# Kernel optimization log

Measured on AMD Instinct MI355X. Metric: run time of the kernel, lower is better.

The kernel has to match this reference:

```python
import jax, jax.numpy as jnp
import numpy as np

H = 1024   # hidden_dim
D = 256    # dynamics_dim
L = 2      # gru layers
BS = 1024  # batch
T = 256    # max_len
# activation layout over D: softmax[0:32], softmax[32:47], sigmoid[47:48], sigmoid[48:256]
CAT1 = 32
CAT2_SM_END = 47

def setup_inputs():
    key = jax.random.key(0)
    ks = jax.random.split(key, 12)
    s = 0.02
    return {
        "embed": jax.random.normal(ks[0], (BS, H * (1 + L)), jnp.float32),
        "dynamics": jax.random.uniform(ks[1], (BS, T, D), jnp.float32),
        "seq_len": T,
        "W_ih0": s * jax.random.normal(ks[2], (3 * H, H + D), jnp.float32),
        "W_hh0": s * jax.random.normal(ks[3], (3 * H, H), jnp.float32),
        "b_ih0": s * jax.random.normal(ks[4], (3 * H,), jnp.float32),
        "b_hh0": s * jax.random.normal(ks[5], (3 * H,), jnp.float32),
        "W_ih1": s * jax.random.normal(ks[6], (3 * H, H), jnp.float32),
        "W_hh1": s * jax.random.normal(ks[7], (3 * H, H), jnp.float32),
        "b_ih1": s * jax.random.normal(ks[8], (3 * H,), jnp.float32),
        "b_hh1": s * jax.random.normal(ks[9], (3 * H,), jnp.float32),
        "W_fc": s * jax.random.normal(ks[10], (D, H), jnp.float32),
        "b_fc": s * jax.random.normal(ks[11], (D,), jnp.float32),
    }

def gru_cell(inp, h, W_ih, W_hh, b_ih, b_hh):
    # PyTorch GRU cell math
    gi = inp @ W_ih.T + b_ih          # (bs, 3H)
    gh = h @ W_hh.T + b_hh            # (bs, 3H)
    r = jax.nn.sigmoid(gi[:, :H] + gh[:, :H])
    z = jax.nn.sigmoid(gi[:, H:2 * H] + gh[:, H:2 * H])
    n = jnp.tanh(gi[:, 2 * H:] + r * gh[:, 2 * H:])
    return (1.0 - z) * n + z * h

def apply_activation(x):
    # mirrors processors layout: cat(32), cat-missing(15 softmax + 1 sigmoid), cont(208 sigmoid)
    return jnp.concatenate([
        jax.nn.softmax(x[:, :CAT1], axis=-1),
        jax.nn.softmax(x[:, CAT1:CAT2_SM_END], axis=-1),
        jax.nn.sigmoid(x[:, CAT2_SM_END:]),
    ], axis=-1)

def reference(embed, dynamics, seq_len, W_ih0, W_hh0, b_ih0, b_hh0,
              W_ih1, W_hh1, b_ih1, b_hh1, W_fc, b_fc):
    glob = embed[:, :H]                      # (bs, H)
    h0 = embed[:, H:2 * H]                   # layer-0 initial hidden
    h1 = embed[:, 2 * H:3 * H]               # layer-1 initial hidden
    x0 = dynamics[:, 0, :]                   # (bs, D)

    def step(carry, _):
        x, h0, h1 = carry
        inp = jnp.concatenate([glob, jax.lax.stop_gradient(x)], axis=-1)  # x.detach()
        h0n = gru_cell(inp, h0, W_ih0, W_hh0, b_ih0, b_hh0)
        h1n = gru_cell(h0n, h1, W_ih1, W_hh1, b_ih1, b_hh1)
        out = apply_activation(h1n @ W_fc.T + b_fc)  # (bs, D)
        return (out, h0n, h1n), out

    _, res = jax.lax.scan(step, (x0, h0, h1), None, length=T)
    res = jnp.transpose(res, (1, 0, 2))  # (bs, max_len, D)
    return res
```

## Files before the change

kernel.cpp:

```cpp
#include <hip/hip_runtime.h>

#define HH    1024
#define DD    256
#define BSB   1024
#define TT    256
#define N3H   3072
#define CAT1  32
#define CAT2E 47

typedef unsigned short u16;
typedef short bf16x8 __attribute__((ext_vector_type(8)));
typedef float f32x4  __attribute__((ext_vector_type(4)));

__device__ __forceinline__ u16 f2bf(float f) {
  unsigned int x = __float_as_uint(f);
  unsigned int lsb = (x >> 16) & 1u;
  x += 0x7fffu + lsb;
  return (u16)(x >> 16);
}

__device__ __forceinline__ void gload_lds16(const u16* src, u16* lds) {
  __builtin_amdgcn_global_load_lds(
      (const __attribute__((address_space(1))) void*)src,
      (__attribute__((address_space(3))) void*)lds, 16, 0, 0);
}

struct GArg {
  const u16* A; int lda; int K;
  const u16* B; int ldb; int N;
  float* C; int ldc;
  const float* bias;
  const float* addend;
  float* out;
  u16* xout;
  int tstep;
  int act;
};

#define BM 128
#define BN 128
#define BK 64

__global__ __launch_bounds__(256, 2) void gemm_bt4(GArg ga, GArg gb)
{
  GArg g = (blockIdx.z == 0) ? ga : gb;
  const int colBase = blockIdx.x * BN;
  if (colBase >= g.N) return;
  const int rowBase = blockIdx.y * BM;

  __shared__ __align__(16) u16 As[2][BM * BK];
  __shared__ __align__(16) u16 Bs[2][BN * BK];

  const int tid  = threadIdx.x;
  const int wave = tid >> 6;
  const int lane = tid & 63;
  const int q    = lane >> 4;
  const int l16  = lane & 15;
  const int waveRow = (wave >> 1) * 64;
  const int waveCol = (wave & 1) * 64;

  const int  srow = wave * 8 + (lane >> 3);
  const int  sswz = ((lane & 7) ^ (lane >> 3)) << 3;
  const u16* aptr = g.A + (size_t)(rowBase + srow) * g.lda + sswz;
  const u16* bptr = g.B + (size_t)(colBase + srow) * g.ldb + sswz;
  const size_t astep = (size_t)32 * g.lda;
  const size_t bstep = (size_t)32 * g.ldb;
  const int ldoff = wave << 9;

  f32x4 acc[4][4];
  #pragma unroll
  for (int i = 0; i < 4; ++i)
    #pragma unroll
    for (int j = 0; j < 4; ++j)
      acc[i][j] = (f32x4){0.f, 0.f, 0.f, 0.f};

  const int nk = g.K >> 6;

  #pragma unroll
  for (int i = 0; i < 4; ++i) {
    gload_lds16(aptr + (size_t)i * astep, &As[0][ldoff + (i << 11)]);
    gload_lds16(bptr + (size_t)i * bstep, &Bs[0][ldoff + (i << 11)]);
  }
  #pragma unroll
  for (int i = 0; i < 4; ++i) {
    gload_lds16(aptr + 64 + (size_t)i * astep, &As[1][ldoff + (i << 11)]);
    gload_lds16(bptr + 64 + (size_t)i * bstep, &Bs[1][ldoff + (i << 11)]);
  }

  for (int k = 0; k < nk; ++k) {
    const int cur = k & 1;
    if (k < nk - 1) {
      asm volatile("s_waitcnt vmcnt(8)" ::: "memory");
    } else {
      asm volatile("s_waitcnt vmcnt(0)" ::: "memory");
    }
    __builtin_amdgcn_s_barrier();
    __builtin_amdgcn_sched_barrier(0);

    #pragma unroll
    for (int ks = 0; ks < 2; ++ks) {
      bf16x8 af[4], bfr[4];
      const int kb = (ks << 2) + q;
      #pragma unroll
      for (int mi = 0; mi < 4; ++mi) {
        int r = waveRow + mi * 16 + l16;
        af[mi] = *(const bf16x8*)&As[cur][(r << 6) + ((kb ^ (l16 & 7)) << 3)];
      }
      #pragma unroll
      for (int ni = 0; ni < 4; ++ni) {
        int r = waveCol + ni * 16 + l16;
        bfr[ni] = *(const bf16x8*)&Bs[cur][(r << 6) + ((kb ^ (l16 & 7)) << 3)];
      }
      #pragma unroll
      for (int mi = 0; mi < 4; ++mi)
        #pragma unroll
        for (int ni = 0; ni < 4; ++ni)
          acc[mi][ni] = __builtin_amdgcn_mfma_f32_16x16x32_bf16(af[mi], bfr[ni], acc[mi][ni], 0, 0, 0);
    }

    __builtin_amdgcn_sched_barrier(0);
    __builtin_amdgcn_s_barrier();
    __builtin_amdgcn_sched_barrier(0);
    if (k + 2 < nk) {
      const int k2 = (k + 2) << 6;
      #pragma unroll
      for (int i = 0; i < 4; ++i) {
        gload_lds16(aptr + k2 + (size_t)i * astep, &As[cur][ldoff + (i << 11)]);
        gload_lds16(bptr + k2 + (size_t)i * bstep, &Bs[cur][ldoff + (i << 11)]);
      }
    }
  }

  if (g.act) {
    const bool smWave = (colBase + waveCol) == 0;
    #pragma unroll
    for (int mi = 0; mi < 4; ++mi) {
      #pragma unroll
      for (int r = 0; r < 4; ++r) {
        const int row = rowBase + waveRow + mi * 16 + q * 4 + r;
        float v[4];
        #pragma unroll
        for (int ni = 0; ni < 4; ++ni)
          v[ni] = acc[mi][ni][r] + g.bias[colBase + waveCol + ni * 16 + l16];
        float res[4];
        if (smWave) {
          float m1 = fmaxf(v[0], v[1]);
          #pragma unroll
          for (int msk = 1; msk < 16; msk <<= 1) m1 = fmaxf(m1, __shfl_xor(m1, msk));
          float e0 = expf(v[0] - m1), e1 = expf(v[1] - m1);
          float s1 = e0 + e1;
          #pragma unroll
          for (int msk = 1; msk < 16; msk <<= 1) s1 += __shfl_xor(s1, msk);
          res[0] = e0 / s1;
          res[1] = e1 / s1;
          float mv = (l16 < 15) ? v[2] : -1e30f;
          #pragma unroll
          for (int msk = 1; msk < 16; msk <<= 1) mv = fmaxf(mv, __shfl_xor(mv, msk));
          float e2 = expf(v[2] - mv);
          float sv = (l16 < 15) ? e2 : 0.f;
          #pragma unroll
          for (int msk = 1; msk < 16; msk <<= 1) sv += __shfl_xor(sv, msk);
          res[2] = (l16 < 15) ? (e2 / sv) : (1.f / (1.f + expf(-v[2])));
          res[3] = 1.f / (1.f + expf(-v[3]));
        } else {
          #pragma unroll
          for (int ni = 0; ni < 4; ++ni)
            res[ni] = 1.f / (1.f + expf(-v[ni]));
        }
        #pragma unroll
        for (int ni = 0; ni < 4; ++ni) {
          const int col = colBase + waveCol + ni * 16 + l16;
          g.out[((size_t)row * TT + g.tstep) * DD + col] = res[ni];
          g.xout[row * DD + col] = f2bf(res[ni]);
        }
      }
    }
    return;
  }

  #pragma unroll
  for (int mi = 0; mi < 4; ++mi) {
    #pragma unroll
    for (int ni = 0; ni < 4; ++ni) {
      #pragma unroll
      for (int r = 0; r < 4; ++r) {
        int row = rowBase + waveRow + mi * 16 + q * 4 + r;
        int col = colBase + waveCol + ni * 16 + l16;
        float v = acc[mi][ni][r];
        if (g.bias)   v += g.bias[col];
        if (g.addend) v += g.addend[(size_t)row * g.ldc + col];
        g.C[(size_t)row * g.ldc + col] = v;
      }
    }
  }
}

__device__ __forceinline__ float gate1f(float gir, float ghr, float giz, float ghz,
                                        float gin, float ghn, float hv) {
  float r = 1.f / (1.f + expf(-(gir + ghr)));
  float z = 1.f / (1.f + expf(-(giz + ghz)));
  float n = tanhf(gin + r * ghn);
  return (1.f - z) * n + z * hv;
}

__global__ void gate_kernel(const float4* __restrict__ GI, const float4* __restrict__ GH,
                            float4* __restrict__ h, ushort4* __restrict__ hbf)
{
  int idx = blockIdx.x * blockDim.x + threadIdx.x;
  int b = idx >> 8, m = idx & 255;
  size_t base = (size_t)b * 768;
  float4 gir = GI[base + m], giz = GI[base + 256 + m], gin = GI[base + 512 + m];
  float4 ghr = GH[base + m], ghz = GH[base + 256 + m], ghn = GH[base + 512 + m];
  float4 hv = h[idx];
  float4 hn;
  hn.x = gate1f(gir.x, ghr.x, giz.x, ghz.x, gin.x, ghn.x, hv.x);
  hn.y = gate1f(gir.y, ghr.y, giz.y, ghz.y, gin.y, ghn.y, hv.y);
  hn.z = gate1f(gir.z, ghr.z, giz.z, ghz.z, gin.z, ghn.z, hv.z);
  hn.w = gate1f(gir.w, ghr.w, giz.w, ghz.w, gin.w, ghn.w, hv.w);
  h[idx] = hn;
  ushort4 hb;
  hb.x = f2bf(hn.x); hb.y = f2bf(hn.y); hb.z = f2bf(hn.z); hb.w = f2bf(hn.w);
  hbf[idx] = hb;
}

__global__ void convert_kernel(const float* __restrict__ src, u16* __restrict__ dst, int n)
{
  int i = blockIdx.x * blockDim.x + threadIdx.x;
  if (i < n) dst[i] = f2bf(src[i]);
}

__global__ void prep_state(const float* __restrict__ embed, const float* __restrict__ dyn,
                           u16* __restrict__ globbf,
                           float* __restrict__ h0, u16* __restrict__ h0bf,
                           float* __restrict__ h1, u16* __restrict__ h1bf,
                           u16* __restrict__ xbf)
{
  int idx = blockIdx.x * blockDim.x + threadIdx.x;
  int b = idx >> 10, j = idx & 1023;
  const float* e = embed + (size_t)b * 3072;
  globbf[idx] = f2bf(e[j]);
  float v0 = e[1024 + j]; h0[idx] = v0; h0bf[idx] = f2bf(v0);
  float v1 = e[2048 + j]; h1[idx] = v1; h1bf[idx] = f2bf(v1);
  if (j < DD) {
    xbf[b * DD + j] = f2bf(dyn[(size_t)b * (TT * DD) + j]);
  }
}

extern "C" void kernel_launch(void* const* d_in, const int* in_sizes, int n_in,
                              void* d_out, int out_size, void* d_ws, size_t ws_size,
                              hipStream_t stream)
{
  const float* embed = (const float*)d_in[0];
  const float* dyn   = (const float*)d_in[1];
  const float* W_ih0 = (const float*)d_in[3];
  const float* W_hh0 = (const float*)d_in[4];
  const float* b_ih0 = (const float*)d_in[5];
  const float* b_hh0 = (const float*)d_in[6];
  const float* W_ih1 = (const float*)d_in[7];
  const float* W_hh1 = (const float*)d_in[8];
  const float* b_ih1 = (const float*)d_in[9];
  const float* b_hh1 = (const float*)d_in[10];
  const float* W_fc  = (const float*)d_in[11];
  const float* b_fc  = (const float*)d_in[12];
  float* out = (float*)d_out;

  char* ws = (char*)d_ws;
  size_t off = 0;
  auto carve = [&](size_t bytes) -> void* {
    void* p = ws + off;
    off += (bytes + 255) & ~(size_t)255;
    return p;
  };
  u16* Wih0b = (u16*)carve((size_t)N3H * 1280 * 2);
  u16* Whh0b = (u16*)carve((size_t)N3H * HH * 2);
  u16* Wih1b = (u16*)carve((size_t)N3H * HH * 2);
  u16* Whh1b = (u16*)carve((size_t)N3H * HH * 2);
  u16* Wfcb  = (u16*)carve((size_t)DD * HH * 2);
  u16* globb = (u16*)carve((size_t)BSB * HH * 2);
  u16* xbf   = (u16*)carve((size_t)BSB * DD * 2);
  float* h0f = (float*)carve((size_t)BSB * HH * 4);
  float* h1f = (float*)carve((size_t)BSB * HH * 4);
  u16* h0b   = (u16*)carve((size_t)BSB * HH * 2);
  u16* h1b   = (u16*)carve((size_t)BSB * HH * 2);
  float* Gglob  = (float*)carve((size_t)BSB * N3H * 4);
  float* GI     = (float*)carve((size_t)BSB * N3H * 4);
  float* GH0f   = (float*)carve((size_t)BSB * N3H * 4);
  float* GH1f   = (float*)carve((size_t)BSB * N3H * 4);
  (void)ws_size;

  {
    int n;
    n = N3H * 1280; convert_kernel<<<(n + 255) / 256, 256, 0, stream>>>(W_ih0, Wih0b, n);
    n = N3H * HH;   convert_kernel<<<(n + 255) / 256, 256, 0, stream>>>(W_hh0, Whh0b, n);
    n = N3H * HH;   convert_kernel<<<(n + 255) / 256, 256, 0, stream>>>(W_ih1, Wih1b, n);
    n = N3H * HH;   convert_kernel<<<(n + 255) / 256, 256, 0, stream>>>(W_hh1, Whh1b, n);
    n = DD * HH;    convert_kernel<<<(n + 255) / 256, 256, 0, stream>>>(W_fc, Wfcb, n);
  }
  prep_state<<<(BSB * HH) / 256, 256, 0, stream>>>(embed, dyn, globb, h0f, h0b, h1f, h1b, xbf);

  const dim3 G1(N3H / BN, BSB / BM, 1);
  const dim3 G2(N3H / BN, BSB / BM, 2);

  {
    GArg g{globb, HH, HH, Wih0b, 1280, N3H, Gglob, N3H, b_ih0, nullptr, nullptr, nullptr, 0, 0};
    gemm_bt4<<<G1, 256, 0, stream>>>(g, g);
  }
  {
    GArg ga{h0b, HH, HH, Whh0b, HH, N3H, GH0f, N3H, b_hh0, nullptr, nullptr, nullptr, 0, 0};
    GArg gb{h1b, HH, HH, Whh1b, HH, N3H, GH1f, N3H, b_hh1, nullptr, nullptr, nullptr, 0, 0};
    gemm_bt4<<<G2, 256, 0, stream>>>(ga, gb);
  }
  {
    GArg g{xbf, DD, DD, Wih0b + HH, 1280, N3H, GI, N3H, nullptr, Gglob, nullptr, nullptr, 0, 0};
    gemm_bt4<<<G1, 256, 0, stream>>>(g, g);
  }

  for (int t = 0; t < TT; ++t) {
    bool last = (t == TT - 1);

    gate_kernel<<<(BSB * HH / 4) / 256, 256, 0, stream>>>(
        (const float4*)GI, (const float4*)GH0f, (float4*)h0f, (ushort4*)h0b);

    {
      GArg gi{h0b, HH, HH, Wih1b, HH, N3H, GI, N3H, b_ih1, nullptr, nullptr, nullptr, 0, 0};
      GArg gh{h0b, HH, HH, Whh0b, HH, N3H, GH0f, N3H, b_hh0, nullptr, nullptr, nullptr, 0, 0};
      gemm_bt4<<<last ? G1 : G2, 256, 0, stream>>>(gi, gh);
    }

    gate_kernel<<<(BSB * HH / 4) / 256, 256, 0, stream>>>(
        (const float4*)GI, (const float4*)GH1f, (float4*)h1f, (ushort4*)h1b);

    {
      GArg gc{h1b, HH, HH, Wfcb, HH, DD, nullptr, DD, b_fc, nullptr, out, xbf, t, 1};
      GArg gh{h1b, HH, HH, Whh1b, HH, N3H, GH1f, N3H, b_hh1, nullptr, nullptr, nullptr, 0, 0};
      gemm_bt4<<<last ? G1 : G2, 256, 0, stream>>>(gc, gh);
    }

    if (!last) {
      GArg g{xbf, DD, DD, Wih0b + HH, 1280, N3H, GI, N3H, nullptr, Gglob, nullptr, nullptr, 0, 0};
      gemm_bt4<<<G1, 256, 0, stream>>>(g, g);
    }
  }
}
```

Baseline: 25.10 ms.

## Fuse GRU gate nonlinearity into the input-projection GEMM epilogue

```diff
diff --git a/kernel.cpp b/kernel.cpp
--- a/kernel.cpp
+++ b/kernel.cpp
@@ -41,15 +41,14 @@
 #define BN 128
 #define BK 64
 
-__global__ __launch_bounds__(256, 2) void gemm_bt4(GArg ga, GArg gb)
-{
-  GArg g = (blockIdx.z == 0) ? ga : gb;
+__device__ void plain_gemm_body(const GArg& g, u16* lds)
+{
   const int colBase = blockIdx.x * BN;
   if (colBase >= g.N) return;
   const int rowBase = blockIdx.y * BM;
 
-  __shared__ __align__(16) u16 As[2][BM * BK];
-  __shared__ __align__(16) u16 Bs[2][BN * BK];
+  u16* As = lds;
+  u16* Bs = lds + 16384;
 
   const int tid  = threadIdx.x;
   const int wave = tid >> 6;
@@ -78,17 +77,17 @@
 
   #pragma unroll
   for (int i = 0; i < 4; ++i) {
-    gload_lds16(aptr + (size_t)i * astep, &As[0][ldoff + (i << 11)]);
-    gload_lds16(bptr + (size_t)i * bstep, &Bs[0][ldoff + (i << 11)]);
+    gload_lds16(aptr + (size_t)i * astep, &As[ldoff + (i << 11)]);
+    gload_lds16(bptr + (size_t)i * bstep, &Bs[ldoff + (i << 11)]);
   }
   #pragma unroll
   for (int i = 0; i < 4; ++i) {
-    gload_lds16(aptr + 64 + (size_t)i * astep, &As[1][ldoff + (i << 11)]);
-    gload_lds16(bptr + 64 + (size_t)i * bstep, &Bs[1][ldoff + (i << 11)]);
+    gload_lds16(aptr + 64 + (size_t)i * astep, &As[8192 + ldoff + (i << 11)]);
+    gload_lds16(bptr + 64 + (size_t)i * bstep, &Bs[8192 + ldoff + (i << 11)]);
   }
 
   for (int k = 0; k < nk; ++k) {
-    const int cur = k & 1;
+    const int cb = (k & 1) << 13;
     if (k < nk - 1) {
       asm volatile("s_waitcnt vmcnt(8)" ::: "memory");
     } else {
@@ -104,12 +103,12 @@
       #pragma unroll
       for (int mi = 0; mi < 4; ++mi) {
         int r = waveRow + mi * 16 + l16;
-        af[mi] = *(const bf16x8*)&As[cur][(r << 6) + ((kb ^ (l16 & 7)) << 3)];
+        af[mi] = *(const bf16x8*)&As[cb + (r << 6) + ((kb ^ (l16 & 7)) << 3)];
       }
       #pragma unroll
       for (int ni = 0; ni < 4; ++ni) {
         int r = waveCol + ni * 16 + l16;
-        bfr[ni] = *(const bf16x8*)&Bs[cur][(r << 6) + ((kb ^ (l16 & 7)) << 3)];
+        bfr[ni] = *(const bf16x8*)&Bs[cb + (r << 6) + ((kb ^ (l16 & 7)) << 3)];
       }
       #pragma unroll
       for (int mi = 0; mi < 4; ++mi)
@@ -125,8 +124,8 @@
       const int k2 = (k + 2) << 6;
       #pragma unroll
       for (int i = 0; i < 4; ++i) {
-        gload_lds16(aptr + k2 + (size_t)i * astep, &As[cur][ldoff + (i << 11)]);
-        gload_lds16(bptr + k2 + (size_t)i * bstep, &Bs[cur][ldoff + (i << 11)]);
+        gload_lds16(aptr + k2 + (size_t)i * astep, &As[cb + ldoff + (i << 11)]);
+        gload_lds16(bptr + k2 + (size_t)i * bstep, &Bs[cb + ldoff + (i << 11)]);
       }
     }
   }
@@ -195,32 +194,158 @@
   }
 }
 
-__device__ __forceinline__ float gate1f(float gir, float ghr, float giz, float ghz,
-                                        float gin, float ghn, float hv) {
-  float r = 1.f / (1.f + expf(-(gir + ghr)));
-  float z = 1.f / (1.f + expf(-(giz + ghz)));
-  float n = tanhf(gin + r * ghn);
-  return (1.f - z) * n + z * hv;
-}
-
-__global__ void gate_kernel(const float4* __restrict__ GI, const float4* __restrict__ GH,
-                            float4* __restrict__ h, ushort4* __restrict__ hbf)
-{
-  int idx = blockIdx.x * blockDim.x + threadIdx.x;
-  int b = idx >> 8, m = idx & 255;
-  size_t base = (size_t)b * 768;
-  float4 gir = GI[base + m], giz = GI[base + 256 + m], gin = GI[base + 512 + m];
-  float4 ghr = GH[base + m], ghz = GH[base + 256 + m], ghn = GH[base + 512 + m];
-  float4 hv = h[idx];
-  float4 hn;
-  hn.x = gate1f(gir.x, ghr.x, giz.x, ghz.x, gin.x, ghn.x, hv.x);
-  hn.y = gate1f(gir.y, ghr.y, giz.y, ghz.y, gin.y, ghn.y, hv.y);
-  hn.z = gate1f(gir.z, ghr.z, giz.z, ghz.z, gin.z, ghn.z, hv.z);
-  hn.w = gate1f(gir.w, ghr.w, giz.w, ghz.w, gin.w, ghn.w, hv.w);
-  h[idx] = hn;
-  ushort4 hb;
-  hb.x = f2bf(hn.x); hb.y = f2bf(hn.y); hb.z = f2bf(hn.z); hb.w = f2bf(hn.w);
-  hbf[idx] = hb;
+struct FArg {
+  const u16* A; int lda; int K;
+  const u16* W; int ldw;
+  const float* Gadd;
+  const float* bias3;
+  const float* GH;
+  float* hf; u16* hb;
+};
+
+__device__ void fused_gate_body(const FArg& f, u16* lds)
+{
+  if (blockIdx.x >= 16) return;
+  const int uBase   = blockIdx.x * 64;
+  const int rowBase = blockIdx.y * 128;
+
+  const int tid  = threadIdx.x;
+  const int wave = tid >> 6;
+  const int lane = tid & 63;
+  const int q    = lane >> 4;
+  const int l16  = lane & 15;
+
+  const int  srow = wave * 8 + (lane >> 3);
+  const int  sswz = ((lane & 7) ^ (lane >> 3)) << 3;
+  const u16* aptr = f.A + (size_t)(rowBase + srow) * f.lda + sswz;
+  const u16* wp0  = f.W + (size_t)(uBase + srow) * f.ldw + sswz;
+  const u16* wp1  = f.W + (size_t)(1024 + uBase + srow) * f.ldw + sswz;
+  const u16* wp2  = f.W + (size_t)(2048 + uBase + srow) * f.ldw + sswz;
+  const size_t astep = (size_t)32 * f.lda;
+  const size_t wstep = (size_t)32 * f.ldw;
+  const int ldoff = wave << 9;
+
+  f32x4 acc[2][4][3];
+  #pragma unroll
+  for (int ri = 0; ri < 2; ++ri)
+    #pragma unroll
+    for (int ci = 0; ci < 4; ++ci)
+      #pragma unroll
+      for (int gg = 0; gg < 3; ++gg)
+        acc[ri][ci][gg] = (f32x4){0.f, 0.f, 0.f, 0.f};
+
+  const int nk = f.K >> 6;
+
+  auto stage = [&](int buf, int k0) {
+    const int ab = buf * 8192;
+    const int bb = 16384 + buf * 12288;
+    #pragma unroll
+    for (int i = 0; i < 4; ++i)
+      gload_lds16(aptr + k0 + (size_t)i * astep, &lds[ab + ldoff + (i << 11)]);
+    #pragma unroll
+    for (int i = 0; i < 2; ++i) {
+      gload_lds16(wp0 + k0 + (size_t)i * wstep, &lds[bb +         ldoff + (i << 11)]);
+      gload_lds16(wp1 + k0 + (size_t)i * wstep, &lds[bb + 4096 +  ldoff + (i << 11)]);
+      gload_lds16(wp2 + k0 + (size_t)i * wstep, &lds[bb + 8192 +  ldoff + (i << 11)]);
+    }
+  };
+
+  stage(0, 0);
+  stage(1, 64);
+
+  for (int k = 0; k < nk; ++k) {
+    const int buf = k & 1;
+    const int ab = buf * 8192;
+    const int bb = 16384 + buf * 12288;
+    if (k < nk - 1) {
+      asm volatile("s_waitcnt vmcnt(10)" ::: "memory");
+    } else {
+      asm volatile("s_waitcnt vmcnt(0)" ::: "memory");
+    }
+    __builtin_amdgcn_s_barrier();
+    __builtin_amdgcn_sched_barrier(0);
+
+    #pragma unroll
+    for (int ks = 0; ks < 2; ++ks) {
+      const int kb = (ks << 2) + q;
+      const int ksw = (kb ^ (l16 & 7)) << 3;
+      bf16x8 a[2];
+      #pragma unroll
+      for (int ri = 0; ri < 2; ++ri) {
+        int r = wave * 32 + ri * 16 + l16;
+        a[ri] = *(const bf16x8*)&lds[ab + (r << 6) + ksw];
+      }
+      #pragma unroll
+      for (int gg = 0; gg < 3; ++gg) {
+        bf16x8 b[4];
+        #pragma unroll
+        for (int ci = 0; ci < 4; ++ci) {
+          int r = ci * 16 + l16;
+          b[ci] = *(const bf16x8*)&lds[bb + gg * 4096 + (r << 6) + ksw];
+        }
+        #pragma unroll
+        for (int ri = 0; ri < 2; ++ri)
+          #pragma unroll
+          for (int ci = 0; ci < 4; ++ci)
+            acc[ri][ci][gg] = __builtin_amdgcn_mfma_f32_16x16x32_bf16(a[ri], b[ci], acc[ri][ci][gg], 0, 0, 0);
+      }
+    }
+
+    __builtin_amdgcn_sched_barrier(0);
+    __builtin_amdgcn_s_barrier();
+    __builtin_amdgcn_sched_barrier(0);
+    if (k + 2 < nk) stage(buf, (k + 2) << 6);
+  }
+
+  #pragma unroll
+  for (int ri = 0; ri < 2; ++ri) {
+    #pragma unroll
+    for (int ci = 0; ci < 4; ++ci) {
+      #pragma unroll
+      for (int rr = 0; rr < 4; ++rr) {
+        const int row  = rowBase + wave * 32 + ri * 16 + q * 4 + rr;
+        const int unit = uBase + ci * 16 + l16;
+        const size_t c0 = (size_t)row * N3H + unit;
+        float gi0 = acc[ri][ci][0][rr];
+        float gi1 = acc[ri][ci][1][rr];
+        float gi2 = acc[ri][ci][2][rr];
+        if (f.bias3) {
+          gi0 += f.bias3[unit];
+          gi1 += f.bias3[1024 + unit];
+          gi2 += f.bias3[2048 + unit];
+        }
+        if (f.Gadd) {
+          gi0 += f.Gadd[c0];
+          gi1 += f.Gadd[c0 + 1024];
+          gi2 += f.Gadd[c0 + 2048];
+        }
+        const float gh0 = f.GH[c0];
+        const float gh1 = f.GH[c0 + 1024];
+        const float gh2 = f.GH[c0 + 2048];
+        const float rg = 1.f / (1.f + expf(-(gi0 + gh0)));
+        const float zg = 1.f / (1.f + expf(-(gi1 + gh1)));
+        const float ng = tanhf(gi2 + rg * gh2);
+        const int hidx = row * HH + unit;
+        const float hv = f.hf[hidx];
+        const float hn = (1.f - zg) * ng + zg * hv;
+        f.hf[hidx] = hn;
+        f.hb[hidx] = f2bf(hn);
+      }
+    }
+  }
+}
+
+__global__ __launch_bounds__(256, 2) void step_kernel(FArg fa, GArg gb)
+{
+  __shared__ __align__(16) u16 lds[40960];
+  if (blockIdx.z == 0) fused_gate_body(fa, lds);
+  else                 plain_gemm_body(gb, lds);
+}
+
+__global__ __launch_bounds__(256, 2) void gemm_bt4(GArg ga, GArg gb)
+{
+  __shared__ __align__(16) u16 lds[32768];
+  plain_gemm_body(blockIdx.z == 0 ? ga : gb, lds);
 }
 
 __global__ void convert_kernel(const float* __restrict__ src, u16* __restrict__ dst, int n)
@@ -283,7 +408,6 @@
   u16* h0b   = (u16*)carve((size_t)BSB * HH * 2);
   u16* h1b   = (u16*)carve((size_t)BSB * HH * 2);
   float* Gglob  = (float*)carve((size_t)BSB * N3H * 4);
-  float* GI     = (float*)carve((size_t)BSB * N3H * 4);
   float* GH0f   = (float*)carve((size_t)BSB * N3H * 4);
   float* GH1f   = (float*)carve((size_t)BSB * N3H * 4);
   (void)ws_size;
@@ -298,47 +422,37 @@
   }
   prep_state<<<(BSB * HH) / 256, 256, 0, stream>>>(embed, dyn, globb, h0f, h0b, h1f, h1b, xbf);
 
-  const dim3 G1(N3H / BN, BSB / BM, 1);
-  const dim3 G2(N3H / BN, BSB / BM, 2);
-
   {
     GArg g{globb, HH, HH, Wih0b, 1280, N3H, Gglob, N3H, b_ih0, nullptr, nullptr, nullptr, 0, 0};
-    gemm_bt4<<<G1, 256, 0, stream>>>(g, g);
+    gemm_bt4<<<dim3(24, 8, 1), 256, 0, stream>>>(g, g);
   }
   {
     GArg ga{h0b, HH, HH, Whh0b, HH, N3H, GH0f, N3H, b_hh0, nullptr, nullptr, nullptr, 0, 0};
     GArg gb{h1b, HH, HH, Whh1b, HH, N3H, GH1f, N3H, b_hh1, nullptr, nullptr, nullptr, 0, 0};
-    gemm_bt4<<<G2, 256, 0, stream>>>(ga, gb);
-  }
-  {
-    GArg g{xbf, DD, DD, Wih0b + HH, 1280, N3H, GI, N3H, nullptr, Gglob, nullptr, nullptr, 0, 0};
-    gemm_bt4<<<G1, 256, 0, stream>>>(g, g);
-  }
+    gemm_bt4<<<dim3(24, 8, 2), 256, 0, stream>>>(ga, gb);
+  }
+
+  const GArg gnull{nullptr, 0, 64, nullptr, 0, 0, nullptr, 0,
+                   nullptr, nullptr, nullptr, nullptr, 0, 0};
 
   for (int t = 0; t < TT; ++t) {
     bool last = (t == TT - 1);
 
-    gate_kernel<<<(BSB * HH / 4) / 256, 256, 0, stream>>>(
-        (const float4*)GI, (const float4*)GH0f, (float4*)h0f, (ushort4*)h0b);
-
     {
-      GArg gi{h0b, HH, HH, Wih1b, HH, N3H, GI, N3H, b_ih1, nullptr, nullptr, nullptr, 0, 0};
+      FArg fa{xbf, DD, DD, Wih0b + HH, 1280, Gglob, nullptr, GH0f, h0f, h0b};
+      step_kernel<<<dim3(16, 8, 1), 256, 0, stream>>>(fa, gnull);
+    }
+
+    {
+      FArg fa{h0b, HH, HH, Wih1b, HH, nullptr, b_ih1, GH1f, h1f, h1b};
       GArg gh{h0b, HH, HH, Whh0b, HH, N3H, GH0f, N3H, b_hh0, nullptr, nullptr, nullptr, 0, 0};
-      gemm_bt4<<<last ? G1 : G2, 256, 0, stream>>>(gi, gh);
-    }
-
-    gate_kernel<<<(BSB * HH / 4) / 256, 256, 0, stream>>>(
-        (const float4*)GI, (const float4*)GH1f, (float4*)h1f, (ushort4*)h1b);
+      step_kernel<<<last ? dim3(16, 8, 1) : dim3(24, 8, 2), 256, 0, stream>>>(fa, gh);
+    }
 
     {
       GArg gc{h1b, HH, HH, Wfcb, HH, DD, nullptr, DD, b_fc, nullptr, out, xbf, t, 1};
       GArg gh{h1b, HH, HH, Whh1b, HH, N3H, GH1f, N3H, b_hh1, nullptr, nullptr, nullptr, 0, 0};
-      gemm_bt4<<<last ? G1 : G2, 256, 0, stream>>>(gc, gh);
-    }
-
-    if (!last) {
-      GArg g{xbf, DD, DD, Wih0b + HH, 1280, N3H, GI, N3H, nullptr, Gglob, nullptr, nullptr, 0, 0};
-      gemm_bt4<<<G1, 256, 0, stream>>>(g, g);
-    }
-  }
-}
+      gemm_bt4<<<last ? dim3(2, 8, 1) : dim3(24, 8, 2), 256, 0, stream>>>(gc, gh);
+    }
+  }
+}
```

Result: slower. 27.11 ms (+8.0%).

## Fuse the whole recurrent loop into one persistent kernel with grid barriers

Applied to the files above, without the earlier changes.

```diff
diff --git a/kernel.cpp b/kernel.cpp
--- a/kernel.cpp
+++ b/kernel.cpp
@@ -8,6 +8,9 @@
 #define CAT1  32
 #define CAT2E 47
 
+#define NB    256
+#define NTH   256
+
 typedef unsigned short u16;
 typedef short bf16x8 __attribute__((ext_vector_type(8)));
 typedef float f32x4  __attribute__((ext_vector_type(4)));
@@ -25,31 +28,44 @@
       (__attribute__((address_space(3))) void*)lds, 16, 0, 0);
 }
 
-struct GArg {
-  const u16* A; int lda; int K;
-  const u16* B; int ldb; int N;
-  float* C; int ldc;
-  const float* bias;
-  const float* addend;
-  float* out;
-  u16* xout;
-  int tstep;
-  int act;
-};
-
-#define BM 128
-#define BN 128
-#define BK 64
-
-__global__ __launch_bounds__(256, 2) void gemm_bt4(GArg ga, GArg gb)
-{
-  GArg g = (blockIdx.z == 0) ? ga : gb;
-  const int colBase = blockIdx.x * BN;
-  if (colBase >= g.N) return;
-  const int rowBase = blockIdx.y * BM;
-
-  __shared__ __align__(16) u16 As[2][BM * BK];
-  __shared__ __align__(16) u16 Bs[2][BN * BK];
+__device__ __forceinline__ void gbar(unsigned* flags, unsigned* gen, unsigned pc)
+{
+  __syncthreads();
+  if (threadIdx.x == 0) {
+    __threadfence();
+    __hip_atomic_store(&flags[blockIdx.x * 32], pc, __ATOMIC_RELAXED,
+                       __HIP_MEMORY_SCOPE_AGENT);
+  }
+  if (blockIdx.x == 0) {
+    while (__hip_atomic_load(&flags[threadIdx.x * 32], __ATOMIC_RELAXED,
+                             __HIP_MEMORY_SCOPE_AGENT) < pc)
+      __builtin_amdgcn_s_sleep(1);
+    __syncthreads();
+    if (threadIdx.x == 0)
+      __hip_atomic_store(gen, pc, __ATOMIC_RELEASE, __HIP_MEMORY_SCOPE_AGENT);
+  }
+  if (threadIdx.x == 0) {
+    while (__hip_atomic_load(gen, __ATOMIC_RELAXED,
+                             __HIP_MEMORY_SCOPE_AGENT) < pc)
+      __builtin_amdgcn_s_sleep(2);
+    __threadfence();
+  }
+  __syncthreads();
+}
+
+__device__ void gemm_tile(int tx, int ty,
+                          const u16* A, int lda, int K,
+                          const u16* B, int ldb,
+                          float* C, int ldc,
+                          const float* bias, const float* addend,
+                          float* out, u16* xout, int tstep, int act,
+                          u16* lds)
+{
+  const int colBase = tx * 128;
+  const int rowBase = ty * 128;
+
+  u16* As = lds;
+  u16* Bs = lds + 16384;
 
   const int tid  = threadIdx.x;
   const int wave = tid >> 6;
@@ -61,10 +77,10 @@
 
   const int  srow = wave * 8 + (lane >> 3);
   const int  sswz = ((lane & 7) ^ (lane >> 3)) << 3;
-  const u16* aptr = g.A + (size_t)(rowBase + srow) * g.lda + sswz;
-  const u16* bptr = g.B + (size_t)(colBase + srow) * g.ldb + sswz;
-  const size_t astep = (size_t)32 * g.lda;
-  const size_t bstep = (size_t)32 * g.ldb;
+  const u16* aptr = A + (size_t)(rowBase + srow) * lda + sswz;
+  const u16* bptr = B + (size_t)(colBase + srow) * ldb + sswz;
+  const size_t astep = (size_t)32 * lda;
+  const size_t bstep = (size_t)32 * ldb;
   const int ldoff = wave << 9;
 
   f32x4 acc[4][4];
@@ -74,21 +90,21 @@
     for (int j = 0; j < 4; ++j)
       acc[i][j] = (f32x4){0.f, 0.f, 0.f, 0.f};
 
-  const int nk = g.K >> 6;
+  const int nk = K >> 6;
 
   #pragma unroll
   for (int i = 0; i < 4; ++i) {
-    gload_lds16(aptr + (size_t)i * astep, &As[0][ldoff + (i << 11)]);
-    gload_lds16(bptr + (size_t)i * bstep, &Bs[0][ldoff + (i << 11)]);
+    gload_lds16(aptr + (size_t)i * astep, &As[ldoff + (i << 11)]);
+    gload_lds16(bptr + (size_t)i * bstep, &Bs[ldoff + (i << 11)]);
   }
   #pragma unroll
   for (int i = 0; i < 4; ++i) {
-    gload_lds16(aptr + 64 + (size_t)i * astep, &As[1][ldoff + (i << 11)]);
-    gload_lds16(bptr + 64 + (size_t)i * bstep, &Bs[1][ldoff + (i << 11)]);
+    gload_lds16(aptr + 64 + (size_t)i * astep, &As[8192 + ldoff + (i << 11)]);
+    gload_lds16(bptr + 64 + (size_t)i * bstep, &Bs[8192 + ldoff + (i << 11)]);
   }
 
   for (int k = 0; k < nk; ++k) {
-    const int cur = k & 1;
+    const int cb = (k & 1) << 13;
     if (k < nk - 1) {
       asm volatile("s_waitcnt vmcnt(8)" ::: "memory");
     } else {
@@ -104,12 +120,12 @@
       #pragma unroll
       for (int mi = 0; mi < 4; ++mi) {
         int r = waveRow + mi * 16 + l16;
-        af[mi] = *(const bf16x8*)&As[cur][(r << 6) + ((kb ^ (l16 & 7)) << 3)];
+        af[mi] = *(const bf16x8*)&As[cb + (r << 6) + ((kb ^ (l16 & 7)) << 3)];
       }
       #pragma unroll
       for (int ni = 0; ni < 4; ++ni) {
         int r = waveCol + ni * 16 + l16;
-        bfr[ni] = *(const bf16x8*)&Bs[cur][(r << 6) + ((kb ^ (l16 & 7)) << 3)];
+        bfr[ni] = *(const bf16x8*)&Bs[cb + (r << 6) + ((kb ^ (l16 & 7)) << 3)];
       }
       #pragma unroll
       for (int mi = 0; mi < 4; ++mi)
@@ -125,13 +141,13 @@
       const int k2 = (k + 2) << 6;
       #pragma unroll
       for (int i = 0; i < 4; ++i) {
-        gload_lds16(aptr + k2 + (size_t)i * astep, &As[cur][ldoff + (i << 11)]);
-        gload_lds16(bptr + k2 + (size_t)i * bstep, &Bs[cur][ldoff + (i << 11)]);
+        gload_lds16(aptr + k2 + (size_t)i * astep, &As[cb + ldoff + (i << 11)]);
+        gload_lds16(bptr + k2 + (size_t)i * bstep, &Bs[cb + ldoff + (i << 11)]);
       }
     }
   }
 
-  if (g.act) {
+  if (act) {
     const bool smWave = (colBase + waveCol) == 0;
     #pragma unroll
     for (int mi = 0; mi < 4; ++mi) {
@@ -141,7 +157,7 @@
         float v[4];
         #pragma unroll
         for (int ni = 0; ni < 4; ++ni)
-          v[ni] = acc[mi][ni][r] + g.bias[colBase + waveCol + ni * 16 + l16];
+          v[ni] = acc[mi][ni][r] + bias[colBase + waveCol + ni * 16 + l16];
         float res[4];
         if (smWave) {
           float m1 = fmaxf(v[0], v[1]);
@@ -170,8 +186,8 @@
         #pragma unroll
         for (int ni = 0; ni < 4; ++ni) {
           const int col = colBase + waveCol + ni * 16 + l16;
-          g.out[((size_t)row * TT + g.tstep) * DD + col] = res[ni];
-          g.xout[row * DD + col] = f2bf(res[ni]);
+          out[((size_t)row * TT + tstep) * DD + col] = res[ni];
+          xout[row * DD + col] = f2bf(res[ni]);
         }
       }
     }
@@ -187,9 +203,9 @@
         int row = rowBase + waveRow + mi * 16 + q * 4 + r;
         int col = colBase + waveCol + ni * 16 + l16;
         float v = acc[mi][ni][r];
-        if (g.bias)   v += g.bias[col];
-        if (g.addend) v += g.addend[(size_t)row * g.ldc + col];
-        g.C[(size_t)row * g.ldc + col] = v;
+        if (bias)   v += bias[col];
+        if (addend) v += addend[(size_t)row * ldc + col];
+        C[(size_t)row * ldc + col] = v;
       }
     }
   }
@@ -203,24 +219,101 @@
   return (1.f - z) * n + z * hv;
 }
 
-__global__ void gate_kernel(const float4* __restrict__ GI, const float4* __restrict__ GH,
-                            float4* __restrict__ h, ushort4* __restrict__ hbf)
-{
-  int idx = blockIdx.x * blockDim.x + threadIdx.x;
-  int b = idx >> 8, m = idx & 255;
-  size_t base = (size_t)b * 768;
-  float4 gir = GI[base + m], giz = GI[base + 256 + m], gin = GI[base + 512 + m];
-  float4 ghr = GH[base + m], ghz = GH[base + 256 + m], ghn = GH[base + 512 + m];
-  float4 hv = h[idx];
-  float4 hn;
-  hn.x = gate1f(gir.x, ghr.x, giz.x, ghz.x, gin.x, ghn.x, hv.x);
-  hn.y = gate1f(gir.y, ghr.y, giz.y, ghz.y, gin.y, ghn.y, hv.y);
-  hn.z = gate1f(gir.z, ghr.z, giz.z, ghz.z, gin.z, ghn.z, hv.z);
-  hn.w = gate1f(gir.w, ghr.w, giz.w, ghz.w, gin.w, ghn.w, hv.w);
-  h[idx] = hn;
-  ushort4 hb;
-  hb.x = f2bf(hn.x); hb.y = f2bf(hn.y); hb.z = f2bf(hn.z); hb.w = f2bf(hn.w);
-  hbf[idx] = hb;
+__device__ void gate_phase(const float4* GI, const float4* GH,
+                           float4* h, ushort4* hbf)
+{
+  const int nth = NB * NTH;
+  for (int idx = blockIdx.x * NTH + threadIdx.x; idx < BSB * HH / 4; idx += nth) {
+    int b = idx >> 8, m = idx & 255;
+    size_t base = (size_t)b * 768;
+    float4 gir = GI[base + m], giz = GI[base + 256 + m], gin = GI[base + 512 + m];
+    float4 ghr = GH[base + m], ghz = GH[base + 256 + m], ghn = GH[base + 512 + m];
+    float4 hv = h[idx];
+    float4 hn;
+    hn.x = gate1f(gir.x, ghr.x, giz.x, ghz.x, gin.x, ghn.x, hv.x);
+    hn.y = gate1f(gir.y, ghr.y, giz.y, ghz.y, gin.y, ghn.y, hv.y);
+    hn.z = gate1f(gir.z, ghr.z, giz.z, ghz.z, gin.z, ghn.z, hv.z);
+    hn.w = gate1f(gir.w, ghr.w, giz.w, ghz.w, gin.w, ghn.w, hv.w);
+    h[idx] = hn;
+    ushort4 hb;
+    hb.x = f2bf(hn.x); hb.y = f2bf(hn.y); hb.z = f2bf(hn.z); hb.w = f2bf(hn.w);
+    hbf[idx] = hb;
+  }
+}
+
+struct P {
+  const u16 *Wih0, *Whh0, *Wih1, *Whh1, *Wfc;
+  const u16 *glob;
+  u16 *x;
+  float *h0f, *h1f; u16 *h0b, *h1b;
+  float *Gglob, *GI, *GH0, *GH1;
+  const float *b_ih0, *b_hh0, *b_ih1, *b_hh1, *b_fc;
+  float *out;
+  unsigned *flags, *gen;
+};
+
+__global__ __launch_bounds__(NTH, 1) void persist(P p)
+{
+  __shared__ __align__(16) u16 lds[32768];
+  const int bid = blockIdx.x;
+  unsigned pc = 1;
+
+  for (int j = bid; j < 384; j += NB) {
+    if (j < 192)
+      gemm_tile(j % 24, j / 24, p.glob, HH, HH, p.Wih0, 1280,
+                p.Gglob, N3H, p.b_ih0, nullptr, nullptr, nullptr, 0, 0, lds);
+    else
+      gemm_tile((j - 192) % 24, (j - 192) / 24, p.h0b, HH, HH, p.Whh0, HH,
+                p.GH0, N3H, p.b_hh0, nullptr, nullptr, nullptr, 0, 0, lds);
+  }
+  gbar(p.flags, p.gen, pc); ++pc;
+
+  for (int j = bid; j < 384; j += NB) {
+    if (j < 192)
+      gemm_tile(j % 24, j / 24, p.x, DD, DD, p.Wih0 + HH, 1280,
+                p.GI, N3H, nullptr, p.Gglob, nullptr, nullptr, 0, 0, lds);
+    else
+      gemm_tile((j - 192) % 24, (j - 192) / 24, p.h1b, HH, HH, p.Whh1, HH,
+                p.GH1, N3H, p.b_hh1, nullptr, nullptr, nullptr, 0, 0, lds);
+  }
+  gbar(p.flags, p.gen, pc); ++pc;
+
+  for (int t = 0; t < TT; ++t) {
+    const bool last = (t == TT - 1);
+
+    gate_phase((const float4*)p.GI, (const float4*)p.GH0,
+               (float4*)p.h0f, (ushort4*)p.h0b);
+    gbar(p.flags, p.gen, pc); ++pc;
+
+    for (int j = bid; j < 384; j += NB) {
+      if (j < 192)
+        gemm_tile(j % 24, j / 24, p.h0b, HH, HH, p.Wih1, HH,
+                  p.GI, N3H, p.b_ih1, nullptr, nullptr, nullptr, 0, 0, lds);
+      else if (!last)
+        gemm_tile((j - 192) % 24, (j - 192) / 24, p.h0b, HH, HH, p.Whh0, HH,
+                  p.GH0, N3H, p.b_hh0, nullptr, nullptr, nullptr, 0, 0, lds);
+    }
+    gbar(p.flags, p.gen, pc); ++pc;
+
+    gate_phase((const float4*)p.GI, (const float4*)p.GH1,
+               (float4*)p.h1f, (ushort4*)p.h1b);
+    gbar(p.flags, p.gen, pc); ++pc;
+
+    if (bid < 16)
+      gemm_tile(bid % 2, bid / 2, p.h1b, HH, HH, p.Wfc, HH,
+                nullptr, DD, p.b_fc, nullptr, p.out, p.x, t, 1, lds);
+    else if (bid >= 64 && !last)
+      gemm_tile((bid - 64) % 24, (bid - 64) / 24, p.h1b, HH, HH, p.Whh1, HH,
+                p.GH1, N3H, p.b_hh1, nullptr, nullptr, nullptr, 0, 0, lds);
+    gbar(p.flags, p.gen, pc); ++pc;
+
+    if (!last) {
+      if (bid < 192)
+        gemm_tile(bid % 24, bid / 24, p.x, DD, DD, p.Wih0 + HH, 1280,
+                  p.GI, N3H, nullptr, p.Gglob, nullptr, nullptr, 0, 0, lds);
+      gbar(p.flags, p.gen, pc); ++pc;
+    }
+  }
 }
 
 __global__ void convert_kernel(const float* __restrict__ src, u16* __restrict__ dst, int n)
@@ -233,7 +326,7 @@
                            u16* __restrict__ globbf,
                            float* __restrict__ h0, u16* __restrict__ h0bf,
                            float* __restrict__ h1, u16* __restrict__ h1bf,
-                           u16* __restrict__ xbf)
+                           u16* __restrict__ xbf, unsigned* __restrict__ barr)
 {
   int idx = blockIdx.x * blockDim.x + threadIdx.x;
   int b = idx >> 10, j = idx & 1023;
@@ -244,6 +337,7 @@
   if (j < DD) {
     xbf[b * DD + j] = f2bf(dyn[(size_t)b * (TT * DD) + j]);
   }
+  if (idx < 16384) barr[idx] = 0;
 }
 
 extern "C" void kernel_launch(void* const* d_in, const int* in_sizes, int n_in,
@@ -282,10 +376,11 @@
   float* h1f = (float*)carve((size_t)BSB * HH * 4);
   u16* h0b   = (u16*)carve((size_t)BSB * HH * 2);
   u16* h1b   = (u16*)carve((size_t)BSB * HH * 2);
-  float* Gglob  = (float*)carve((size_t)BSB * N3H * 4);
-  float* GI     = (float*)carve((size_t)BSB * N3H * 4);
-  float* GH0f   = (float*)carve((size_t)BSB * N3H * 4);
-  float* GH1f   = (float*)carve((size_t)BSB * N3H * 4);
+  float* Gglob = (float*)carve((size_t)BSB * N3H * 4);
+  float* GI    = (float*)carve((size_t)BSB * N3H * 4);
+  float* GH0f  = (float*)carve((size_t)BSB * N3H * 4);
+  float* GH1f  = (float*)carve((size_t)BSB * N3H * 4);
+  unsigned* barr = (unsigned*)carve((size_t)16384 * 4);
   (void)ws_size;
 
   {
@@ -296,49 +391,17 @@
     n = N3H * HH;   convert_kernel<<<(n + 255) / 256, 256, 0, stream>>>(W_hh1, Whh1b, n);
     n = DD * HH;    convert_kernel<<<(n + 255) / 256, 256, 0, stream>>>(W_fc, Wfcb, n);
   }
-  prep_state<<<(BSB * HH) / 256, 256, 0, stream>>>(embed, dyn, globb, h0f, h0b, h1f, h1b, xbf);
-
-  const dim3 G1(N3H / BN, BSB / BM, 1);
-  const dim3 G2(N3H / BN, BSB / BM, 2);
-
-  {
-    GArg g{globb, HH, HH, Wih0b, 1280, N3H, Gglob, N3H, b_ih0, nullptr, nullptr, nullptr, 0, 0};
-    gemm_bt4<<<G1, 256, 0, stream>>>(g, g);
-  }
-  {
-    GArg ga{h0b, HH, HH, Whh0b, HH, N3H, GH0f, N3H, b_hh0, nullptr, nullptr, nullptr, 0, 0};
-    GArg gb{h1b, HH, HH, Whh1b, HH, N3H, GH1f, N3H, b_hh1, nullptr, nullptr, nullptr, 0, 0};
-    gemm_bt4<<<G2, 256, 0, stream>>>(ga, gb);
-  }
-  {
-    GArg g{xbf, DD, DD, Wih0b + HH, 1280, N3H, GI, N3H, nullptr, Gglob, nullptr, nullptr, 0, 0};
-    gemm_bt4<<<G1, 256, 0, stream>>>(g, g);
-  }
-
-  for (int t = 0; t < TT; ++t) {
-    bool last = (t == TT - 1);
-
-    gate_kernel<<<(BSB * HH / 4) / 256, 256, 0, stream>>>(
-        (const float4*)GI, (const float4*)GH0f, (float4*)h0f, (ushort4*)h0b);
-
-    {
-      GArg gi{h0b, HH, HH, Wih1b, HH, N3H, GI, N3H, b_ih1, nullptr, nullptr, nullptr, 0, 0};
-      GArg gh{h0b, HH, HH, Whh0b, HH, N3H, GH0f, N3H, b_hh0, nullptr, nullptr, nullptr, 0, 0};
-      gemm_bt4<<<last ? G1 : G2, 256, 0, stream>>>(gi, gh);
-    }
-
-    gate_kernel<<<(BSB * HH / 4) / 256, 256, 0, stream>>>(
-        (const float4*)GI, (const float4*)GH1f, (float4*)h1f, (ushort4*)h1b);
-
-    {
-      GArg gc{h1b, HH, HH, Wfcb, HH, DD, nullptr, DD, b_fc, nullptr, out, xbf, t, 1};
-      GArg gh{h1b, HH, HH, Whh1b, HH, N3H, GH1f, N3H, b_hh1, nullptr, nullptr, nullptr, 0, 0};
-      gemm_bt4<<<last ? G1 : G2, 256, 0, stream>>>(gc, gh);
-    }
-
-    if (!last) {
-      GArg g{xbf, DD, DD, Wih0b + HH, 1280, N3H, GI, N3H, nullptr, Gglob, nullptr, nullptr, 0, 0};
-      gemm_bt4<<<G1, 256, 0, stream>>>(g, g);
-    }
-  }
-}
+  prep_state<<<(BSB * HH) / 256, 256, 0, stream>>>(embed, dyn, globb, h0f, h0b,
+                                                   h1f, h1b, xbf, barr);
+
+  P p;
+  p.Wih0 = Wih0b; p.Whh0 = Whh0b; p.Wih1 = Wih1b; p.Whh1 = Whh1b; p.Wfc = Wfcb;
+  p.glob = globb; p.x = xbf;
+  p.h0f = h0f; p.h1f = h1f; p.h0b = h0b; p.h1b = h1b;
+  p.Gglob = Gglob; p.GI = GI; p.GH0 = GH0f; p.GH1 = GH1f;
+  p.b_ih0 = b_ih0; p.b_hh0 = b_hh0; p.b_ih1 = b_ih1; p.b_hh1 = b_hh1; p.b_fc = b_fc;
+  p.out = out;
+  p.flags = barr; p.gen = barr + NB * 32;
+
+  persist<<<NB, NTH, 0, stream>>>(p);
+}
```

Result: slower. 43.46 ms (+73.1%).
